# Performance work log

Hardware: AMD Instinct MI355X
Metric: run time of the kernel (lower is better)

## Reference

```python
import jax, jax.numpy as jnp
import numpy as np
from jax import lax

C = 64   # channels
R = 2    # SKM expansion ratio
M = 4    # number of dilated convs
EPS = 1e-6


def conv3_dilated(x, w, b, d):
    # 3x3 conv, dilation d, padding d (same spatial size)
    y = lax.conv_general_dilated(x, w, (1, 1), [(d, d), (d, d)],
                                 rhs_dilation=(d, d),
                                 dimension_numbers=('NCHW', 'OIHW', 'NCHW'))
    return y + b[None, :, None, None]


def ln2d(x, g, b):
    # LayerNorm over channel dim at each spatial position (NAFNet LayerNorm2d)
    mu = x.mean(1, keepdims=True)
    var = x.var(1, keepdims=True)
    return (x - mu) / jnp.sqrt(var + EPS) * g[None, :, None, None] + b[None, :, None, None]


def skm(x, dw, db, c1w, c1b, pw):
    # dw: [M,C,C,3,3], db: [M,C], c1w: [R*C,C], c1b: [R*C], pw: [R*C, M*C]
    D = jnp.stack([conv3_dilated(x, dw[i], db[i], 2 * (i + 1)) for i in range(M)])  # [M,B,C,H,W]
    Z = D.sum(0).mean((-2, -1))                      # [B,C] global avg pool of summed branches
    S = jax.nn.relu(Z @ c1w.T + c1b)                 # [B,R*C]
    Sw = jax.nn.softmax((S @ pw).reshape(-1, M, C), axis=-1)  # [B,M,C], softmax over C
    return jnp.einsum('mbchw,bmc->bchw', D, Sw)      # weighted sum of branches


def setup_inputs() -> dict:
    key = jax.random.key(0)
    ks = jax.random.split(key, 24)
    B, H, W = 4, 96, 256
    sc = 0.05
    inp = {
        'x_l': jax.random.normal(ks[0], (B, C, H, W), jnp.float32),
        'x_r': jax.random.normal(ks[1], (B, C, H, W), jnp.float32),
        'lnl_g': jnp.ones((C,), jnp.float32),
        'lnl_b': jnp.zeros((C,), jnp.float32),
        'lnr_g': jnp.ones((C,), jnp.float32),
        'lnr_b': jnp.zeros((C,), jnp.float32),
        'l_dw': jax.random.normal(ks[2], (M, C, C, 3, 3), jnp.float32) * sc,
        'l_db': jax.random.normal(ks[3], (M, C), jnp.float32) * sc,
        'l_c1w': jax.random.normal(ks[4], (R * C, C), jnp.float32) * sc,
        'l_c1b': jax.random.normal(ks[5], (R * C,), jnp.float32) * sc,
        'l_pw': jax.random.normal(ks[6], (R * C, M * C), jnp.float32) * sc,
        'r_dw': jax.random.normal(ks[7], (M, C, C, 3, 3), jnp.float32) * sc,
        'r_db': jax.random.normal(ks[8], (M, C), jnp.float32) * sc,
        'r_c1w': jax.random.normal(ks[9], (R * C, C), jnp.float32) * sc,
        'r_c1b': jax.random.normal(ks[10], (R * C,), jnp.float32) * sc,
        'r_pw': jax.random.normal(ks[11], (R * C, M * C), jnp.float32) * sc,
        'l2w': jax.random.normal(ks[12], (C, C), jnp.float32) * sc,
        'l2b': jax.random.normal(ks[13], (C,), jnp.float32) * sc,
        'r2w': jax.random.normal(ks[14], (C, C), jnp.float32) * sc,
        'r2b': jax.random.normal(ks[15], (C,), jnp.float32) * sc,
        'beta': jax.random.normal(ks[16], (1, C, 1, 1), jnp.float32) * sc,
        'gamma': jax.random.normal(ks[17], (1, C, 1, 1), jnp.float32) * sc,
    }
    return inp


def reference(x_l, x_r, lnl_g, lnl_b, lnr_g, lnr_b,
              l_dw, l_db, l_c1w, l_c1b, l_pw,
              r_dw, r_db, r_c1w, r_c1b, r_pw,
              l2w, l2b, r2w, r2b, beta, gamma):
    scale = C ** (-0.5)
    Ql = skm(ln2d(x_l, lnl_g, lnl_b), l_dw, l_db, l_c1w, l_c1b, l_pw).transpose(0, 2, 3, 1)  # [B,H,W,C]
    Qr = skm(ln2d(x_r, lnr_g, lnr_b), r_dw, r_db, r_c1w, r_c1b, r_pw).transpose(0, 2, 3, 1)  # [B,H,W,C]
    Vl = (jnp.einsum('bchw,dc->bdhw', x_l, l2w) + l2b[None, :, None, None]).transpose(0, 2, 3, 1)
    Vr = (jnp.einsum('bchw,dc->bdhw', x_r, r2w) + r2b[None, :, None, None]).transpose(0, 2, 3, 1)
    attn = jnp.einsum('bhwc,bhvc->bhwv', Ql, Qr) * scale  # shared score matrix [B,H,W,W]
    F_r2l = jnp.einsum('bhwv,bhvc->bhwc', jax.nn.softmax(attn, axis=-1), Vr).transpose(0, 3, 1, 2)
    F_l2r = jnp.einsum('bhwv,bhwc->bhvc', jax.nn.softmax(attn, axis=-2), Vl).transpose(0, 3, 1, 2)
    return x_l + F_r2l * beta, x_r + F_l2r * gamma
```

## Files before the change

kernel.cpp:

```cpp
#include <hip/hip_runtime.h>
#include <hip/hip_bf16.h>
#include <cstdint>

constexpr int NB = 4;
constexpr int NC = 64;
constexpr int NH = 96;
constexpr int NW = 256;
constexpr int HWp = NH * NW;
constexpr float EPS = 1e-6f;

typedef __attribute__((ext_vector_type(8))) short short8;
typedef __attribute__((ext_vector_type(4))) short short4t;
typedef __attribute__((ext_vector_type(4))) float f32x4;

static __device__ __forceinline__ short f2bf(float f) {
    __hip_bfloat16 h = __float2bfloat16(f);
    return *reinterpret_cast<short*>(&h);
}

__global__ __launch_bounds__(256) void k_lnv(const float* __restrict__ x_l,
                                             const float* __restrict__ x_r,
                                             const float* __restrict__ gl,
                                             const float* __restrict__ bl,
                                             const float* __restrict__ gr,
                                             const float* __restrict__ br,
                                             short* __restrict__ XBl,
                                             short* __restrict__ XBr,
                                             float* __restrict__ R,
                                             const float* __restrict__ w2l,
                                             const float* __restrict__ b2l,
                                             const float* __restrict__ w2r,
                                             const float* __restrict__ b2r,
                                             short* __restrict__ VL,
                                             short* __restrict__ VR) {
    __shared__ float smem[8704];
    const int h = blockIdx.y, sideb = blockIdx.z;
    const int side = sideb >> 2, b = sideb & 3;
    const int t = threadIdx.x;

    if (blockIdx.x == 4) {
        const float* x = side ? x_r : x_l;
        const float* g = side ? gr : gl;
        const float* bta = side ? br : bl;
        short* XB = side ? XBr : XBl;
        float* xm = smem;

        const float* xp = x + ((size_t)b * NC * NH + h) * NW + t;
        float v[64];
        float s = 0.f, sq = 0.f;
#pragma unroll
        for (int c = 0; c < 64; ++c) {
            float tv = xp[(size_t)c * HWp];
            v[c] = tv; s += tv; sq += tv * tv;
        }
        float mu = s * (1.f / 64.f);
        float var = sq * (1.f / 64.f) - mu * mu;
        float rs = rsqrtf(var + EPS);
#pragma unroll
        for (int c = 0; c < 64; ++c) v[c] = (v[c] - mu) * rs * g[c] + bta[c];

#pragma unroll
        for (int chunk = 0; chunk < 4; ++chunk) {
            short8 s0, s1;
#pragma unroll
            for (int j = 0; j < 8; ++j) {
                s0[j] = f2bf(v[chunk * 16 + j]);
                s1[j] = f2bf(v[chunk * 16 + 8 + j]);
            }
            short* xb = XB + (((size_t)(b * 4 + chunk) * NH + h) * NW + t) * 16;
            *(short8*)xb = s0;
            *(short8*)(xb + 8) = s1;
        }

#pragma unroll
        for (int p = 0; p < 2; ++p) {
            const int cbase = p * 32;
            __syncthreads();
#pragma unroll
            for (int c = 0; c < 32; ++c)
                xm[c * 256 + (((t >> 2) ^ (c & 7)) << 2) + (t & 3)] = v[cbase + c];
            __syncthreads();
            const int cc = t & 31, q = t >> 5;
            float rsum = 0.f;
            float4 fs0 = {0,0,0,0}, fs1 = {0,0,0,0}, ls0 = {0,0,0,0}, ls1 = {0,0,0,0};
#pragma unroll
            for (int i = 0; i < 8; ++i) {
                int j4 = q * 8 + i;
                float4 f = *(const float4*)&xm[cc * 256 + ((j4 ^ (cc & 7)) << 2)];
                rsum += (f.x + f.y) + (f.z + f.w);
                if (i == 0) fs0 = f;
                if (i == 1) fs1 = f;
                if (i == 6) ls0 = f;
                if (i == 7) ls1 = f;
            }
            __syncthreads();
            xm[cc * 8 + q] = rsum;
            if (q == 7) {
                *(float4*)&xm[256 + cc * 8] = ls0;
                *(float4*)&xm[256 + cc * 8 + 4] = ls1;
            }
            __syncthreads();
            if (t < 32) {
                const int c = t;
                float full = 0.f;
#pragma unroll
                for (int q2 = 0; q2 < 8; ++q2) full += xm[c * 8 + q2];
                float h0 = xm[256 + c * 8 + 0], h1 = xm[256 + c * 8 + 1];
                float h2 = xm[256 + c * 8 + 2], h3 = xm[256 + c * 8 + 3];
                float h4 = xm[256 + c * 8 + 4], h5 = xm[256 + c * 8 + 5];
                float h6 = xm[256 + c * 8 + 6], h7 = xm[256 + c * 8 + 7];
                float e2 = fs0.x + fs0.y;
                float e4 = e2 + fs0.z + fs0.w;
                float e6 = e4 + fs1.x + fs1.y;
                float e8 = e6 + fs1.z + fs1.w;
                float r2 = h6 + h7;
                float r4 = (h4 + h5) + r2;
                float r6 = r4 + (h2 + h3);
                float r8 = r6 + (h0 + h1);
                float* Rp = R + ((size_t)(sideb * 64 + cbase + c) * NH + h) * 9;
                Rp[0] = full; Rp[1] = e2; Rp[2] = e4; Rp[3] = e6; Rp[4] = e8;
                Rp[5] = r2;  Rp[6] = r4; Rp[7] = r6; Rp[8] = r8;
            }
        }
    } else {
        const int wt = blockIdx.x;
        const float* x  = side ? x_r : x_l;
        const float* w2 = side ? w2r : w2l;
        const float* b2 = side ? b2r : b2l;
        short* VT = side ? VR : VL;
        const int lane = t & 63, q = t >> 6;
        float* xs  = smem;
        float* w2t = smem + 4352;
        int w0 = wt * 64;
        const float* src = x + (size_t)(b * 64) * HWp + h * NW + w0;
        for (int idx = t; idx < 4096; idx += 256) {
            int ci = idx >> 6, col = idx & 63;
            xs[ci * 68 + col] = src[(size_t)ci * HWp + col];
        }
        for (int idx = t; idx < 4096; idx += 256) {
            int co = idx >> 6, ci = idx & 63;
            w2t[ci * 68 + co] = w2[co * 64 + ci];
        }
        __syncthreads();

        const int pl0 = (lane & 15) * 4;
        const int c0 = q * 16 + (lane >> 4) * 4;
        f32x4 a4[4];
#pragma unroll
        for (int cc = 0; cc < 4; ++cc) {
            float bb = b2[c0 + cc];
            a4[cc] = (f32x4){bb, bb, bb, bb};
        }
        for (int ci = 0; ci < 64; ++ci) {
            f32x4 xv = *(const f32x4*)(xs + ci * 68 + pl0);
            f32x4 wv = *(const f32x4*)(w2t + ci * 68 + c0);
            a4[0] += xv * wv[0];
            a4[1] += xv * wv[1];
            a4[2] += xv * wv[2];
            a4[3] += xv * wv[3];
        }
        __syncthreads();
#pragma unroll
        for (int cc = 0; cc < 4; ++cc)
            *(f32x4*)(xs + (c0 + cc) * 68 + pl0) = a4[cc];
        __syncthreads();
        {
            int s = t & 63, g2 = t >> 6;
            int u = (s >> 2) + 16 * (s & 3);
#pragma unroll
            for (int cc = 0; cc < 16; ++cc) {
                int ch = g2 * 16 + cc;
                VT[((size_t)(b * 64 + ch) * NH + h) * NW + w0 + s] = f2bf(xs[ch * 68 + u]);
            }
        }
    }
}

__global__ __launch_bounds__(128) void k_comb(const float* __restrict__ R,
                                              float* __restrict__ T) {
    int x = blockIdx.x;
    int side = x >> 8, rem = x & 255, b = rem >> 6, ci = rem & 63;
    __shared__ float rp[NH][9];
    int t = threadIdx.x;
    const float* src = R + (size_t)x * NH * 9;
    for (int i = t; i < NH * 9; i += 128) ((float*)rp)[i] = src[i];
    __syncthreads();
    if (t < 36) {
        int m = t / 9, kh = (t % 9) / 3, kw = t % 3;
        int d = 2 * (m + 1);
        int r0 = (kh == 2) ? d : 0;
        int r1 = (kh == 0) ? NH - d : NH;
        float s = 0.f;
        for (int r = r0; r < r1; ++r) {
            float rowv = rp[r][0];
            if (kw == 0) rowv -= rp[r][5 + m];
            else if (kw == 2) rowv -= rp[r][1 + m];
            s += rowv;
        }
        T[side * 9216 + (b * 4 + m) * 576 + ci * 9 + kh * 3 + kw] = s;
    }
}

__global__ __launch_bounds__(256) void k_z(const float* __restrict__ T,
                                           const float* __restrict__ l_dw,
                                           const float* __restrict__ r_dw,
                                           const float* __restrict__ l_db,
                                           const float* __restrict__ r_db,
                                           float* __restrict__ Z) {
    int x = blockIdx.x;
    int side = x >> 8, bc = x & 255;
    int b = bc >> 6, c = bc & 63;
    const float* dw = side ? r_dw : l_dw;
    const float* db = side ? r_db : l_db;
    int t = threadIdx.x, lane = t & 63, m = t >> 6;
    const float* wp = dw + (size_t)(m * 64 + c) * 576;
    const float* tp = T + side * 9216 + (size_t)(b * 4 + m) * 576;
    float s = 0.f;
    for (int j = lane; j < 576; j += 64) s += wp[j] * tp[j];
#pragma unroll
    for (int o = 32; o; o >>= 1) s += __shfl_xor(s, o, 64);
    __shared__ float red[4];
    if (lane == 0) red[m] = s;
    __syncthreads();
    if (t == 0) {
        float z = (red[0] + red[1]) + (red[2] + red[3]);
        float bias = db[c] + db[64 + c] + db[128 + c] + db[192 + c];
        Z[x] = z * (1.f / (float)HWp) + bias;
    }
}

__global__ __launch_bounds__(256) void k_sel2(const float* __restrict__ Z,
                                              const float* __restrict__ l_db,
                                              const float* __restrict__ r_db,
                                              const float* __restrict__ l_c1w,
                                              const float* __restrict__ r_c1w,
                                              const float* __restrict__ l_c1b,
                                              const float* __restrict__ r_c1b,
                                              const float* __restrict__ l_pw,
                                              const float* __restrict__ r_pw,
                                              float* __restrict__ Sw,
                                              float* __restrict__ Qb) {
    int x = blockIdx.x;
    int side = x >> 2;
    const float* db  = side ? r_db  : l_db;
    const float* c1w = side ? r_c1w : l_c1w;
    const float* c1b = side ? r_c1b : l_c1b;
    const float* pw  = side ? r_pw  : l_pw;
    int t = threadIdx.x, lane = t & 63, wv = t >> 6;
    __shared__ float zs[64], ss[128], sw[256];
    __shared__ float cw[128 * 64];
    if (t < 64) zs[t] = Z[x * 64 + t];
    for (int i = t; i < 8192; i += 256) cw[i] = c1w[i];
    __syncthreads();
    if (t < 128) {
        float s = c1b[t];
        const float* wrow = cw + t * 64;
        for (int c = 0; c < 64; ++c) s += zs[c] * wrow[c];
        ss[t] = fmaxf(s, 0.f);
    }
    __syncthreads();
    float p = 0.f;
    for (int j = 0; j < 128; ++j) p += ss[j] * pw[j * 256 + t];
    float mx = p;
#pragma unroll
    for (int o = 32; o; o >>= 1) mx = fmaxf(mx, __shfl_xor(mx, o, 64));
    float e = __expf(p - mx);
    float sum = e;
#pragma unroll
    for (int o = 32; o; o >>= 1) sum += __shfl_xor(sum, o, 64);
    float swv = e / sum;
    Sw[(x * 4 + wv) * 64 + lane] = swv;
    sw[wv * 64 + lane] = swv;
    __syncthreads();
    if (t < 64) {
        float qb = sw[t] * db[t] + sw[64 + t] * db[64 + t]
                 + sw[128 + t] * db[128 + t] + sw[192 + t] * db[192 + t];
        Qb[x * 64 + t] = qb;
    }
}

__global__ __launch_bounds__(256) void k_fold(const float* __restrict__ l_dw,
                                              const float* __restrict__ r_dw,
                                              const float* __restrict__ Sw,
                                              short* __restrict__ WB) {
    int bx = blockIdx.x;
    int side = (bx >= 2304) ? 1 : 0;
    int idx = (bx - side * 2304) * 256 + threadIdx.x;
    const float* dw = side ? r_dw : l_dw;
    short* wbs = WB + (size_t)side * 589824;
    int kk = idx & 31;
    int co = (idx >> 5) & 63;
    int rest = idx >> 11;
    int tpair = rest % 18;
    int bc = rest / 18;
    int chunk = bc & 3, b = bc >> 2;
    int tpl = kk >> 4, cil = kk & 15;
    int tap = 2 * tpair + tpl;
    int m = tap / 9, k9 = tap % 9;
    int ci = chunk * 16 + cil;
    float val = Sw[((side * 4 + b) * 4 + m) * 64 + co]
              * dw[(size_t)((m * 64 + co) * 64 + ci) * 9 + k9];
    wbs[idx] = f2bf(val);
}

__global__ __launch_bounds__(256) void k_convm(const short* __restrict__ XBl,
                                               const short* __restrict__ XBr,
                                               const short* __restrict__ WBa,
                                               const float* __restrict__ QBa,
                                               short* __restrict__ QLs,
                                               short* __restrict__ QRs) {
    const int wt = blockIdx.x, h = blockIdx.y;
    const int side = blockIdx.z >> 2, b = blockIdx.z & 3;
    const short* XB = side ? XBr : XBl;
    const short* WB = WBa + (size_t)side * 589824;
    const float* Qb = QBa + side * 256;
    short* Qs = side ? QRs : QLs;
    const int t = threadIdx.x;
    const int lane = t & 63, wave = t >> 6;
    const int g = lane >> 4, ln15 = lane & 15;
    __shared__ short tile[2 * 9 * 144 * 8];

    f32x4 acc[2][4];
    {
        float qb[4];
#pragma unroll
        for (int nt = 0; nt < 4; ++nt) qb[nt] = Qb[b * 64 + nt * 16 + ln15];
#pragma unroll
        for (int mt = 0; mt < 2; ++mt)
#pragma unroll
            for (int nt = 0; nt < 4; ++nt)
                acc[mt][nt] = (f32x4){qb[nt], qb[nt], qb[nt], qb[nt]};
    }
    const int w0 = wt * 128;
    const int laneelem = (wave * 32 + ln15) * 8;
    const int halfoff = (g & 1) * (9 * 144 * 8);
    const int tsel = g >> 1;

    short8 pv[6][2];
    auto LOADC = [&](int chunk) {
        const short* src = XB + (size_t)(b * 4 + chunk) * NH * NW * 16;
#pragma unroll
        for (int i = 0; i < 6; ++i) {
            const int slot = t + i * 256;
            const bool live = (i < 5) || (t < 16);
            short8 z = {0, 0, 0, 0, 0, 0, 0, 0};
            pv[i][0] = z; pv[i][1] = z;
            if (live) {
                int r = slot / 144, col = slot % 144;
                int gh = h + 2 * r - 8;
                int gw = w0 - 8 + col;
                if (gh >= 0 && gh < NH && gw >= 0 && gw < NW) {
                    const short* p = src + ((size_t)gh * NW + gw) * 16;
                    pv[i][0] = *(const short8*)p;
                    pv[i][1] = *(const short8*)(p + 8);
                }
            }
        }
    };

    LOADC(0);
    for (int chunk = 0; chunk < 4; ++chunk) {
        __builtin_amdgcn_s_barrier();
        __builtin_amdgcn_sched_barrier(0);
#pragma unroll
        for (int i = 0; i < 6; ++i) {
            const int slot = t + i * 256;
            const bool live = (i < 5) || (t < 16);
            if (live) {
                *(short8*)(tile + slot * 8) = pv[i][0];
                *(short8*)(tile + (9 * 144 + slot) * 8) = pv[i][1];
            }
        }
        if (chunk < 3) LOADC(chunk + 1);
        asm volatile("s_waitcnt lgkmcnt(0)" ::: "memory");
        __builtin_amdgcn_s_barrier();
        __builtin_amdgcn_sched_barrier(0);

        const short* wbase = WB + (size_t)((b * 4 + chunk) * 18) * 2048 + ln15 * 32 + g * 8;
#pragma unroll
        for (int tp = 0; tp < 18; ++tp) {
            const int ta = 2 * tp, tb = ta + 1;
            const int ma = ta / 9, k9a = ta % 9;
            const int mb = tb / 9, k9b = tb % 9;
            const int offA = ((4 + (ma + 1) * (k9a / 3 - 1)) * 144 + 8 + 2 * (ma + 1) * (k9a % 3 - 1)) * 8;
            const int offB = ((4 + (mb + 1) * (k9b / 3 - 1)) * 144 + 8 + 2 * (mb + 1) * (k9b % 3 - 1)) * 8;
            const int aoff = (tsel ? offB : offA) + laneelem + halfoff;
            const short* bp = wbase + (size_t)tp * 2048;
            short8 b0 = *(const short8*)(bp);
            short8 b1 = *(const short8*)(bp + 512);
            short8 b2 = *(const short8*)(bp + 1024);
            short8 b3 = *(const short8*)(bp + 1536);
            const short* ap = tile + aoff;
            short8 a0 = *(const short8*)(ap);
            short8 a1 = *(const short8*)(ap + 128);
            acc[0][0] = __builtin_amdgcn_mfma_f32_16x16x32_bf16(a0, b0, acc[0][0], 0, 0, 0);
            acc[0][1] = __builtin_amdgcn_mfma_f32_16x16x32_bf16(a0, b1, acc[0][1], 0, 0, 0);
            acc[0][2] = __builtin_amdgcn_mfma_f32_16x16x32_bf16(a0, b2, acc[0][2], 0, 0, 0);
            acc[0][3] = __builtin_amdgcn_mfma_f32_16x16x32_bf16(a0, b3, acc[0][3], 0, 0, 0);
            acc[1][0] = __builtin_amdgcn_mfma_f32_16x16x32_bf16(a1, b0, acc[1][0], 0, 0, 0);
            acc[1][1] = __builtin_amdgcn_mfma_f32_16x16x32_bf16(a1, b1, acc[1][1], 0, 0, 0);
            acc[1][2] = __builtin_amdgcn_mfma_f32_16x16x32_bf16(a1, b2, acc[1][2], 0, 0, 0);
            acc[1][3] = __builtin_amdgcn_mfma_f32_16x16x32_bf16(a1, b3, acc[1][3], 0, 0, 0);
        }
    }
#pragma unroll
    for (int mt = 0; mt < 2; ++mt) {
        int px = w0 + wave * 32 + mt * 16 + g * 4;
#pragma unroll
        for (int j = 0; j < 4; ++j) {
            short* qp = Qs + ((size_t)(b * NH + h) * NW + px + j) * 64 + ln15;
            qp[0]  = f2bf(acc[mt][0][j]);
            qp[16] = f2bf(acc[mt][1][j]);
            qp[32] = f2bf(acc[mt][2][j]);
            qp[48] = f2bf(acc[mt][3][j]);
        }
    }
}

__global__ __launch_bounds__(128, 2) void k_attn(const short* __restrict__ QL,
                                                 const short* __restrict__ QR,
                                                 const short* __restrict__ VL,
                                                 const short* __restrict__ VR,
                                                 const float* __restrict__ x_l,
                                                 const float* __restrict__ x_r,
                                                 const float* __restrict__ beta,
                                                 const float* __restrict__ gamma,
                                                 float* __restrict__ out_all) {
    const int bx = blockIdx.x, h = blockIdx.y;
    const int side = blockIdx.z >> 2, b = blockIdx.z & 3;
    constexpr size_t PLANE = (size_t)NB * NC * NH * NW;
    const short* Qa  = side ? QR : QL;
    const short* Qbp = side ? QL : QR;
    const short* VT  = side ? VL : VR;
    const float* xres = side ? x_r : x_l;
    const float* scl  = side ? gamma : beta;
    float* out = out_all + (side ? PLANE : 0);

    const int t = threadIdx.x, lane = t & 63, wave = t >> 6;
    const int q = lane >> 4, c15 = lane & 15;
    __shared__ __align__(16) short PB[2][32 * 72];
    short* pb = PB[wave];

    const int wbase = bx * 64 + wave * 32;
    const short* qabase = Qa + ((size_t)(b * NH + h) * NW + wbase) * 64;
    const short* qbbase = Qbp + ((size_t)(b * NH + h) * NW) * 64;

    short8 afrag[2][2];
#pragma unroll
    for (int mt = 0; mt < 2; ++mt)
#pragma unroll
        for (int kk = 0; kk < 2; ++kk)
            afrag[mt][kk] = *(const short8*)(qabase + (mt * 16 + c15) * 64 + kk * 32 + q * 8);

    f32x4 osum[2][4];
#pragma unroll
    for (int mt = 0; mt < 2; ++mt)
#pragma unroll
        for (int nt = 0; nt < 4; ++nt) osum[mt][nt] = (f32x4){0.f, 0.f, 0.f, 0.f};
    float mrow[8], lrow[8];
#pragma unroll
    for (int i = 0; i < 8; ++i) { mrow[i] = -1e30f; lrow[i] = 0.f; }

    for (int vt = 0; vt < 4; ++vt) {
        f32x4 s[2][4];
#pragma unroll
        for (int mt = 0; mt < 2; ++mt)
#pragma unroll
            for (int nt = 0; nt < 4; ++nt) s[mt][nt] = (f32x4){0.f, 0.f, 0.f, 0.f};
#pragma unroll
        for (int kk = 0; kk < 2; ++kk) {
            short8 bq[4];
#pragma unroll
            for (int nt = 0; nt < 4; ++nt)
                bq[nt] = *(const short8*)(qbbase + (size_t)(vt * 64 + nt * 16 + c15) * 64 + kk * 32 + q * 8);
#pragma unroll
            for (int mt = 0; mt < 2; ++mt)
#pragma unroll
                for (int nt = 0; nt < 4; ++nt)
                    s[mt][nt] = __builtin_amdgcn_mfma_f32_16x16x32_bf16(afrag[mt][kk], bq[nt], s[mt][nt], 0, 0, 0);
        }
#pragma unroll
        for (int mt = 0; mt < 2; ++mt)
#pragma unroll
            for (int nt = 0; nt < 4; ++nt)
#pragma unroll
                for (int r = 0; r < 4; ++r) s[mt][nt][r] *= 0.125f;
        float al[8];
#pragma unroll
        for (int mt = 0; mt < 2; ++mt)
#pragma unroll
            for (int r = 0; r < 4; ++r) {
                float m0 = fmaxf(fmaxf(s[mt][0][r], s[mt][1][r]), fmaxf(s[mt][2][r], s[mt][3][r]));
#pragma unroll
                for (int msk = 1; msk < 16; msk <<= 1) m0 = fmaxf(m0, __shfl_xor(m0, msk, 64));
                int i = mt * 4 + r;
                float mn = fmaxf(mrow[i], m0);
                al[i] = __expf(mrow[i] - mn);
                mrow[i] = mn;
            }
#pragma unroll
        for (int mt = 0; mt < 2; ++mt)
#pragma unroll
            for (int r = 0; r < 4; ++r) {
                int i = mt * 4 + r;
                float m = mrow[i];
                float p0 = __expf(s[mt][0][r] - m);
                float p1 = __expf(s[mt][1][r] - m);
                float p2 = __expf(s[mt][2][r] - m);
                float p3 = __expf(s[mt][3][r] - m);
                short4t pk = {f2bf(p0), f2bf(p1), f2bf(p2), f2bf(p3)};
                *(short4t*)(pb + (mt * 16 + q * 4 + r) * 72 + c15 * 4) = pk;
                float lsv = (p0 + p1) + (p2 + p3);
#pragma unroll
                for (int msk = 1; msk < 16; msk <<= 1) lsv += __shfl_xor(lsv, msk, 64);
                lrow[i] = lrow[i] * al[i] + lsv;
            }
#pragma unroll
        for (int mt = 0; mt < 2; ++mt)
#pragma unroll
            for (int nt = 0; nt < 4; ++nt)
#pragma unroll
                for (int r = 0; r < 4; ++r) osum[mt][nt][r] *= al[mt * 4 + r];
#pragma unroll
        for (int kk = 0; kk < 2; ++kk) {
            short8 ap[2], bv[4];
#pragma unroll
            for (int mt = 0; mt < 2; ++mt)
                ap[mt] = *(const short8*)(pb + (mt * 16 + c15) * 72 + kk * 32 + q * 8);
#pragma unroll
            for (int nt = 0; nt < 4; ++nt)
                bv[nt] = *(const short8*)(VT + ((size_t)(b * 64 + nt * 16 + c15) * NH + h) * NW + vt * 64 + kk * 32 + q * 8);
#pragma unroll
            for (int mt = 0; mt < 2; ++mt)
#pragma unroll
                for (int nt = 0; nt < 4; ++nt)
                    osum[mt][nt] = __builtin_amdgcn_mfma_f32_16x16x32_bf16(ap[mt], bv[nt], osum[mt][nt], 0, 0, 0);
        }
    }
    float linv[8];
#pragma unroll
    for (int i = 0; i < 8; ++i) linv[i] = 1.f / lrow[i];
#pragma unroll
    for (int nt = 0; nt < 4; ++nt) {
        int c = nt * 16 + c15;
        float bv = scl[c];
        size_t pbase = ((size_t)(b * 64 + c) * NH + h) * NW + wbase;
#pragma unroll
        for (int mt = 0; mt < 2; ++mt)
#pragma unroll
            for (int r = 0; r < 4; ++r) {
                size_t o = pbase + mt * 16 + q * 4 + r;
                out[o] = xres[o] + osum[mt][nt][r] * linv[mt * 4 + r] * bv;
            }
    }
}

extern "C" void kernel_launch(void* const* d_in, const int* in_sizes, int n_in,
                              void* d_out, int out_size, void* d_ws, size_t ws_size,
                              hipStream_t stream) {
    const float* x_l   = (const float*)d_in[0];
    const float* x_r   = (const float*)d_in[1];
    const float* lnl_g = (const float*)d_in[2];
    const float* lnl_b = (const float*)d_in[3];
    const float* lnr_g = (const float*)d_in[4];
    const float* lnr_b = (const float*)d_in[5];
    const float* l_dw  = (const float*)d_in[6];
    const float* l_db  = (const float*)d_in[7];
    const float* l_c1w = (const float*)d_in[8];
    const float* l_c1b = (const float*)d_in[9];
    const float* l_pw  = (const float*)d_in[10];
    const float* r_dw  = (const float*)d_in[11];
    const float* r_db  = (const float*)d_in[12];
    const float* r_c1w = (const float*)d_in[13];
    const float* r_c1b = (const float*)d_in[14];
    const float* r_pw  = (const float*)d_in[15];
    const float* l2w   = (const float*)d_in[16];
    const float* l2b   = (const float*)d_in[17];
    const float* r2w   = (const float*)d_in[18];
    const float* r2b   = (const float*)d_in[19];
    const float* beta  = (const float*)d_in[20];
    const float* gamma = (const float*)d_in[21];
    float* out = (float*)d_out;

    constexpr size_t PLANE = (size_t)NB * NC * NH * NW;
    float* ws = (float*)d_ws;
    short* XBl = (short*)ws;         ws += PLANE / 2;
    short* XBr = (short*)ws;         ws += PLANE / 2;
    short* QLs = (short*)ws;         ws += PLANE / 2;
    short* QRs = (short*)ws;         ws += PLANE / 2;
    short* VLs = (short*)ws;         ws += PLANE / 2;
    short* VRs = (short*)ws;         ws += PLANE / 2;
    short* WB  = (short*)ws;         ws += 589824;
    float* Rb  = ws;                 ws += 442368;
    float* Tb  = ws;                 ws += 18432;
    float* SW  = ws;                 ws += 2048;
    float* QB  = ws;                 ws += 512;
    float* Zb  = ws;                 ws += 512;

    dim3 blk(256);
    k_lnv   <<<dim3(5, NH, 2 * NB), blk, 0, stream>>>(x_l, x_r, lnl_g, lnl_b, lnr_g, lnr_b,
                                                      XBl, XBr, Rb,
                                                      l2w, l2b, r2w, r2b, VLs, VRs);
    k_comb  <<<dim3(512), dim3(128), 0, stream>>>(Rb, Tb);
    k_z     <<<dim3(512), blk, 0, stream>>>(Tb, l_dw, r_dw, l_db, r_db, Zb);
    k_sel2  <<<dim3(8), blk, 0, stream>>>(Zb, l_db, r_db, l_c1w, r_c1w,
                                          l_c1b, r_c1b, l_pw, r_pw, SW, QB);
    k_fold  <<<dim3(4608), blk, 0, stream>>>(l_dw, r_dw, SW, WB);
    k_convm <<<dim3(2, NH, 2 * NB), blk, 0, stream>>>(XBl, XBr, WB, QB, QLs, QRs);
    k_attn  <<<dim3(4, NH, 2 * NB), dim3(128), 0, stream>>>(QLs, QRs, VLs, VRs,
                                                            x_l, x_r, beta, gamma, out);
}
```

Before: 374.4 us.

## Split conv output channels across waves and drop register prefetch of input tiles

The dilated-conv kernel now gives each wave a 16-channel output slice over all 128 pixels instead of a 32-pixel strip over all 64 channels. Each wave therefore loads one weight fragment and eight LDS activation fragments per step, rather than four weight fragments and two activation fragments. The register double-buffered prefetch of the next input chunk is replaced by a simple synchronous load-to-LDS loop with __syncthreads. This cuts global weight traffic per wave and register pressure, but raises LDS reads and loses the overlap of global loads with MFMA work.

```diff
diff --git a/kernel.cpp b/kernel.cpp
--- a/kernel.cpp
+++ b/kernel.cpp
@@ -320,63 +320,38 @@
     const int g = lane >> 4, ln15 = lane & 15;
     __shared__ short tile[2 * 9 * 144 * 8];
 
-    f32x4 acc[2][4];
+    f32x4 acc[8];
     {
-        float qb[4];
-#pragma unroll
-        for (int nt = 0; nt < 4; ++nt) qb[nt] = Qb[b * 64 + nt * 16 + ln15];
-#pragma unroll
-        for (int mt = 0; mt < 2; ++mt)
-#pragma unroll
-            for (int nt = 0; nt < 4; ++nt)
-                acc[mt][nt] = (f32x4){qb[nt], qb[nt], qb[nt], qb[nt]};
+        float qb = Qb[b * 64 + wave * 16 + ln15];
+#pragma unroll
+        for (int mt = 0; mt < 8; ++mt)
+            acc[mt] = (f32x4){qb, qb, qb, qb};
     }
     const int w0 = wt * 128;
-    const int laneelem = (wave * 32 + ln15) * 8;
     const int halfoff = (g & 1) * (9 * 144 * 8);
     const int tsel = g >> 1;
 
-    short8 pv[6][2];
-    auto LOADC = [&](int chunk) {
+    for (int chunk = 0; chunk < 4; ++chunk) {
+        __syncthreads();
         const short* src = XB + (size_t)(b * 4 + chunk) * NH * NW * 16;
-#pragma unroll
-        for (int i = 0; i < 6; ++i) {
-            const int slot = t + i * 256;
-            const bool live = (i < 5) || (t < 16);
-            short8 z = {0, 0, 0, 0, 0, 0, 0, 0};
-            pv[i][0] = z; pv[i][1] = z;
-            if (live) {
-                int r = slot / 144, col = slot % 144;
-                int gh = h + 2 * r - 8;
-                int gw = w0 - 8 + col;
-                if (gh >= 0 && gh < NH && gw >= 0 && gw < NW) {
-                    const short* p = src + ((size_t)gh * NW + gw) * 16;
-                    pv[i][0] = *(const short8*)p;
-                    pv[i][1] = *(const short8*)(p + 8);
-                }
-            }
-        }
-    };
-
-    LOADC(0);
-    for (int chunk = 0; chunk < 4; ++chunk) {
-        __builtin_amdgcn_s_barrier();
-        __builtin_amdgcn_sched_barrier(0);
-#pragma unroll
-        for (int i = 0; i < 6; ++i) {
-            const int slot = t + i * 256;
-            const bool live = (i < 5) || (t < 16);
-            if (live) {
-                *(short8*)(tile + slot * 8) = pv[i][0];
-                *(short8*)(tile + (9 * 144 + slot) * 8) = pv[i][1];
-            }
-        }
-        if (chunk < 3) LOADC(chunk + 1);
-        asm volatile("s_waitcnt lgkmcnt(0)" ::: "memory");
-        __builtin_amdgcn_s_barrier();
-        __builtin_amdgcn_sched_barrier(0);
-
-        const short* wbase = WB + (size_t)((b * 4 + chunk) * 18) * 2048 + ln15 * 32 + g * 8;
+        for (int slot = t; slot < 9 * 144; slot += 256) {
+            int r = slot / 144, col = slot % 144;
+            int gh = h + 2 * r - 8;
+            int gw = w0 - 8 + col;
+            short8 v0 = {0, 0, 0, 0, 0, 0, 0, 0};
+            short8 v1 = {0, 0, 0, 0, 0, 0, 0, 0};
+            if (gh >= 0 && gh < NH && gw >= 0 && gw < NW) {
+                const short* p = src + ((size_t)gh * NW + gw) * 16;
+                v0 = *(const short8*)p;
+                v1 = *(const short8*)(p + 8);
+            }
+            *(short8*)(tile + slot * 8) = v0;
+            *(short8*)(tile + (9 * 144 + slot) * 8) = v1;
+        }
+        __syncthreads();
+
+        const short* wbase = WB + (size_t)((b * 4 + chunk) * 18) * 2048
+                           + wave * 512 + ln15 * 32 + g * 8;
 #pragma unroll
         for (int tp = 0; tp < 18; ++tp) {
             const int ta = 2 * tp, tb = ta + 1;
@@ -384,35 +359,34 @@
             const int mb = tb / 9, k9b = tb % 9;
             const int offA = ((4 + (ma + 1) * (k9a / 3 - 1)) * 144 + 8 + 2 * (ma + 1) * (k9a % 3 - 1)) * 8;
             const int offB = ((4 + (mb + 1) * (k9b / 3 - 1)) * 144 + 8 + 2 * (mb + 1) * (k9b % 3 - 1)) * 8;
-            const int aoff = (tsel ? offB : offA) + laneelem + halfoff;
-            const short* bp = wbase + (size_t)tp * 2048;
-            short8 b0 = *(const short8*)(bp);
-            short8 b1 = *(const short8*)(bp + 512);
-            short8 b2 = *(const short8*)(bp + 1024);
-            short8 b3 = *(const short8*)(bp + 1536);
+            const int aoff = (tsel ? offB : offA) + ln15 * 8 + halfoff;
+            short8 bf = *(const short8*)(wbase + (size_t)tp * 2048);
             const short* ap = tile + aoff;
             short8 a0 = *(const short8*)(ap);
             short8 a1 = *(const short8*)(ap + 128);
-            acc[0][0] = __builtin_amdgcn_mfma_f32_16x16x32_bf16(a0, b0, acc[0][0], 0, 0, 0);
-            acc[0][1] = __builtin_amdgcn_mfma_f32_16x16x32_bf16(a0, b1, acc[0][1], 0, 0, 0);
-            acc[0][2] = __builtin_amdgcn_mfma_f32_16x16x32_bf16(a0, b2, acc[0][2], 0, 0, 0);
-            acc[0][3] = __builtin_amdgcn_mfma_f32_16x16x32_bf16(a0, b3, acc[0][3], 0, 0, 0);
-            acc[1][0] = __builtin_amdgcn_mfma_f32_16x16x32_bf16(a1, b0, acc[1][0], 0, 0, 0);
-            acc[1][1] = __builtin_amdgcn_mfma_f32_16x16x32_bf16(a1, b1, acc[1][1], 0, 0, 0);
-            acc[1][2] = __builtin_amdgcn_mfma_f32_16x16x32_bf16(a1, b2, acc[1][2], 0, 0, 0);
-            acc[1][3] = __builtin_amdgcn_mfma_f32_16x16x32_bf16(a1, b3, acc[1][3], 0, 0, 0);
-        }
-    }
-#pragma unroll
-    for (int mt = 0; mt < 2; ++mt) {
-        int px = w0 + wave * 32 + mt * 16 + g * 4;
+            short8 a2 = *(const short8*)(ap + 256);
+            short8 a3 = *(const short8*)(ap + 384);
+            short8 a4 = *(const short8*)(ap + 512);
+            short8 a5 = *(const short8*)(ap + 640);
+            short8 a6 = *(const short8*)(ap + 768);
+            short8 a7 = *(const short8*)(ap + 896);
+            acc[0] = __builtin_amdgcn_mfma_f32_16x16x32_bf16(a0, bf, acc[0], 0, 0, 0);
+            acc[1] = __builtin_amdgcn_mfma_f32_16x16x32_bf16(a1, bf, acc[1], 0, 0, 0);
+            acc[2] = __builtin_amdgcn_mfma_f32_16x16x32_bf16(a2, bf, acc[2], 0, 0, 0);
+            acc[3] = __builtin_amdgcn_mfma_f32_16x16x32_bf16(a3, bf, acc[3], 0, 0, 0);
+            acc[4] = __builtin_amdgcn_mfma_f32_16x16x32_bf16(a4, bf, acc[4], 0, 0, 0);
+            acc[5] = __builtin_amdgcn_mfma_f32_16x16x32_bf16(a5, bf, acc[5], 0, 0, 0);
+            acc[6] = __builtin_amdgcn_mfma_f32_16x16x32_bf16(a6, bf, acc[6], 0, 0, 0);
+            acc[7] = __builtin_amdgcn_mfma_f32_16x16x32_bf16(a7, bf, acc[7], 0, 0, 0);
+        }
+    }
+#pragma unroll
+    for (int mt = 0; mt < 8; ++mt) {
+        int px = w0 + mt * 16 + g * 4;
 #pragma unroll
         for (int j = 0; j < 4; ++j) {
-            short* qp = Qs + ((size_t)(b * NH + h) * NW + px + j) * 64 + ln15;
-            qp[0]  = f2bf(acc[mt][0][j]);
-            qp[16] = f2bf(acc[mt][1][j]);
-            qp[32] = f2bf(acc[mt][2][j]);
-            qp[48] = f2bf(acc[mt][3][j]);
+            Qs[((size_t)(b * NH + h) * NW + px + j) * 64 + wave * 16 + ln15]
+                = f2bf(acc[mt][j]);
         }
     }
 }
```

Result: faster. 315.5 us (-15.7%).
